# Kernel optimization log

Hardware: AMD Instinct MI355X
Metric: run time of the kernel (lower is better)

## Reference

```python
import jax, jax.numpy as jnp
import numpy as np

T = 64      # simulation_length
B = 128     # batch
D = 2048    # flattened input dim / axons per core
N = 2048    # neurons per core
L = 4       # number of cores (chain, latency = index)
OUT = 1024  # number of output_sources


def setup_inputs() -> dict:
    key = jax.random.key(0)
    k0, k1, k2, k3 = jax.random.split(key, 4)
    x = jax.random.uniform(k0, (B, D), dtype=jnp.float32)          # rate-coded input in [0,1)
    # core_params[l] = core_matrix.transpose() -> shape [N, A]; scaled for sane membrane dynamics
    W = jax.random.normal(k1, (L, N, D), dtype=jnp.float32) * 0.05
    thresholds = jnp.ones((L,), dtype=jnp.float32)
    # axon_sources: per-core irregular gather indices into previous core's neurons (input for l=0)
    axon_idx = jax.random.randint(k2, (L, D), 0, D, dtype=jnp.int32)
    out_idx = jax.random.randint(k3, (OUT,), 0, N, dtype=jnp.int32)
    return dict(x=x, W=W, thresholds=thresholds, axon_idx=axon_idx,
                out_idx=out_idx, simulation_length=T)


def _ideal_spike_scan(avg, thr, T):
    """Per-cycle: m += avg; spike = (m > thr); m[m > thr] -= thr.  avg: [B, N]."""
    def step(m, _):
        m = m + avg
        s = (m > thr).astype(m.dtype)
        return m - thr * s, s
    _, spikes = jax.lax.scan(step, jnp.zeros_like(avg), None, length=T)
    return spikes  # [T, B, N]


def reference(x, W, thresholds, axon_idx, out_idx, simulation_length):
    T = simulation_length
    L = W.shape[0]
    # generate_input_spike_train: x replicated across all cycles -> cache[-1]
    prev = jnp.broadcast_to(x, (T,) + x.shape)  # [T, B, D]
    for l in range(L):
        # get_signal_tensor: gather axon source signals for every cycle
        gathered = prev[:, :, axon_idx[l]]                    # [T, B, A]
        # per-cycle matmul: torch.matmul(core_params, sig.T).T == sig @ W[l].T
        val = jnp.einsum('tba,na->tbn', gathered, W[l])       # [T, B, N]
        avg = val.mean(axis=0)                                # avg_values [B, N]
        # ideal membrane integrate + threshold-reset recurrence -> out spike train
        prev = _ideal_spike_scan(avg, thresholds[l], T)       # [T, B, N]
    # output_signals: sum of output-source spikes over all cycles
    return prev[:, :, out_idx].sum(axis=0)                    # [B, OUT]
```

## Files before the change

### kernel.cpp

```cpp
#include <hip/hip_runtime.h>

#define BB   128
#define DD   2048
#define NN   2048
#define LL   4
#define OUTN 1024
#define JBQ  32
#define NDIG 5

typedef double double4v __attribute__((ext_vector_type(4)));
typedef int    int4v    __attribute__((ext_vector_type(4)));
typedef char   char4v   __attribute__((ext_vector_type(4)));

__global__ __launch_bounds__(256) void gather0_kernel(
    const float* __restrict__ x, const int* __restrict__ idx0,
    float* __restrict__ At)
{
    int i = blockIdx.x * 256 + threadIdx.x;
    int k = i >> 7;
    int b = i & 127;
    At[i] = x[b * DD + idx0[k]];
}

__global__ __launch_bounds__(256) void wdig5_kernel(
    const float* __restrict__ W1, signed char* __restrict__ Wd)
{
    const size_t DP = (size_t)NN * DD;
    size_t i  = (size_t)blockIdx.x * 256 + threadIdx.x;
    int    l  = (int)(i / (DP / 4));
    size_t e4 = i - (size_t)l * (DP / 4);
    int n = (int)(e4 >> 9);
    int k = (int)(e4 & 511) * 4;
    float4 w = *(const float4*)(W1 + (size_t)l * DP + (size_t)n * DD + k);
    const float wv[4] = {w.x, w.y, w.z, w.w};
    unsigned long long V[4];
    #pragma unroll
    for (int e = 0; e < 4; ++e)
        V[e] = (unsigned long long)(__double2ll_rn((double)wv[e] * 0x1p33)
                                    + (1LL << 34));
    signed char* base = Wd + (size_t)l * 5 * DP
                      + (size_t)(n >> 5) * 65536 + (size_t)(k >> 6) * 2048
                      + (n & 31) * 64 + (k & 63);
    #pragma unroll
    for (int j = 0; j < NDIG; ++j) {
        char4v p = { (char)((V[0] >> (7 * j)) & 127),
                     (char)((V[1] >> (7 * j)) & 127),
                     (char)((V[2] >> (7 * j)) & 127),
                     (char)((V[3] >> (7 * j)) & 127) };
        *(char4v*)(base + (size_t)j * DP) = p;
    }
}

__global__ __launch_bounds__(256) void gather8_kernel(
    const signed char* __restrict__ c8T, const int* __restrict__ idx,
    signed char* __restrict__ g8T)
{
    int i = blockIdx.x * 256 + threadIdx.x;
    int b = i >> 9;
    int k = (i & 511) * 4;
    int4 id = *(const int4*)(idx + k);
    const signed char* row = c8T + (size_t)b * DD;
    char4v v = { row[id.x], row[id.y], row[id.z], row[id.w] };
    *(char4v*)(g8T + (size_t)(k >> 6) * 8192 + b * 64 + (k & 63)) = v;
}

__global__ __launch_bounds__(256, 2) void layer_kernel(
    const float* __restrict__ srcT,
    const int*   __restrict__ idx,
    const float* __restrict__ Wl,
    const float* __restrict__ thresholds, int l,
    const int*   __restrict__ Tptr,
    float* __restrict__ dst, signed char* __restrict__ c8T, int isLast)
{
    __shared__ double red[4 * 64 * 8];

    const int t    = threadIdx.x;
    const int wq   = t >> 6;
    const int lane = t & 63;
    const int q    = lane >> 4;
    const int c    = lane & 15;

    const int g     = blockIdx.x;
    const int btile = (g >> 3) & 7;
    const int nsup  = (g & 7) | ((g >> 6) << 3);
    const int n0    = nsup * 32;
    const int bcol  = btile * 16 + c;

    double4v pr = {0., 0., 0., 0.}, pcv = {0., 0., 0., 0.};
    pr  = __builtin_amdgcn_mfma_f64_16x16x4f64(0.25 * (double)c, 1.0, pr, 0, 0, 0);
    pcv = __builtin_amdgcn_mfma_f64_16x16x4f64(0.25, (double)c, pcv, 0, 0, 0);
    int rowD[4], colD[4];
    #pragma unroll
    for (int r = 0; r < 4; ++r) {
        rowD[r] = (int)(pr[r] + 0.25);
        colD[r] = (int)(pcv[r] + 0.25);
    }

    double4v acc0[4] = {{0.,0.,0.,0.},{0.,0.,0.,0.},{0.,0.,0.,0.},{0.,0.,0.,0.}};
    double4v acc1[4] = {{0.,0.,0.,0.},{0.,0.,0.,0.},{0.,0.,0.,0.},{0.,0.,0.,0.}};

    const int    kbase = wq * (DD / 4);
    const float* wb0   = Wl + (size_t)(n0 + c) * DD + kbase + 4 * q;
    const float* wb1   = wb0 + (size_t)16 * DD;
    const int*   ibase = idx ? (idx + kbase + 4 * q) : nullptr;

    float4 wv0[4], wv1[4];
    float4 sv[4];
    int4   iv[4];

    #pragma unroll
    for (int p = 0; p < 4; ++p) {
        wv0[p] = *(const float4*)(wb0 + 16 * p);
        wv1[p] = *(const float4*)(wb1 + 16 * p);
    }
    #pragma unroll
    for (int p = 0; p < 4; ++p) {
        int r0, r1, r2, r3;
        if (ibase) {
            int4 iv0 = *(const int4*)(ibase + 16 * p);
            r0 = iv0.x; r1 = iv0.y; r2 = iv0.z; r3 = iv0.w;
        } else {
            int kb = kbase + 16 * p + 4 * q;
            r0 = kb; r1 = kb + 1; r2 = kb + 2; r3 = kb + 3;
        }
        sv[p].x = srcT[(size_t)r0 * BB + bcol];
        sv[p].y = srcT[(size_t)r1 * BB + bcol];
        sv[p].z = srcT[(size_t)r2 * BB + bcol];
        sv[p].w = srcT[(size_t)r3 * BB + bcol];
    }
    if (ibase) {
        #pragma unroll
        for (int p = 0; p < 4; ++p) iv[p] = *(const int4*)(ibase + 16 * (4 + p));
    }

    for (int u = 0; u < JBQ / 4; ++u) {
        #pragma unroll
        for (int gg = 0; gg < 4; ++gg) {
            float4 w0 = wv0[gg];
            float4 w1 = wv1[gg];
            float4 s  = sv[gg];

            int jn = 4 * u + 4 + gg; if (jn > JBQ - 1) jn = JBQ - 1;
            wv0[gg] = *(const float4*)(wb0 + 16 * jn);
            wv1[gg] = *(const float4*)(wb1 + 16 * jn);

            int r0, r1, r2, r3;
            if (ibase) {
                int4 ivv = iv[gg];
                r0 = ivv.x; r1 = ivv.y; r2 = ivv.z; r3 = ivv.w;
            } else {
                int kb = kbase + 16 * jn + 4 * q;
                r0 = kb; r1 = kb + 1; r2 = kb + 2; r3 = kb + 3;
            }
            sv[gg].x = srcT[(size_t)r0 * BB + bcol];
            sv[gg].y = srcT[(size_t)r1 * BB + bcol];
            sv[gg].z = srcT[(size_t)r2 * BB + bcol];
            sv[gg].w = srcT[(size_t)r3 * BB + bcol];

            if (ibase) {
                int jm = 4 * u + 8 + gg; if (jm > JBQ - 1) jm = JBQ - 1;
                iv[gg] = *(const int4*)(ibase + 16 * jm);
            }

            acc0[0] = __builtin_amdgcn_mfma_f64_16x16x4f64((double)w0.x, (double)s.x, acc0[0], 0, 0, 0);
            acc1[0] = __builtin_amdgcn_mfma_f64_16x16x4f64((double)w1.x, (double)s.x, acc1[0], 0, 0, 0);
            acc0[1] = __builtin_amdgcn_mfma_f64_16x16x4f64((double)w0.y, (double)s.y, acc0[1], 0, 0, 0);
            acc1[1] = __builtin_amdgcn_mfma_f64_16x16x4f64((double)w1.y, (double)s.y, acc1[1], 0, 0, 0);
            acc0[2] = __builtin_amdgcn_mfma_f64_16x16x4f64((double)w0.z, (double)s.z, acc0[2], 0, 0, 0);
            acc1[2] = __builtin_amdgcn_mfma_f64_16x16x4f64((double)w1.z, (double)s.z, acc1[2], 0, 0, 0);
            acc0[3] = __builtin_amdgcn_mfma_f64_16x16x4f64((double)w0.w, (double)s.w, acc0[3], 0, 0, 0);
            acc1[3] = __builtin_amdgcn_mfma_f64_16x16x4f64((double)w1.w, (double)s.w, acc1[3], 0, 0, 0);
        }
    }

    double4v a0 = (acc0[0] + acc0[1]) + (acc0[2] + acc0[3]);
    double4v a1 = (acc1[0] + acc1[1]) + (acc1[2] + acc1[3]);

    {
        double* my = red + ((size_t)wq * 64 + lane) * 8;
        #pragma unroll
        for (int r = 0; r < 4; ++r) { my[r] = a0[r]; my[4 + r] = a1[r]; }
    }
    __syncthreads();
    if (wq < 2) {
        const int off = wq * 4;
        double a[4];
        #pragma unroll
        for (int r = 0; r < 4; ++r) {
            a[r] =  red[((size_t)0 * 64 + lane) * 8 + off + r];
            a[r] += red[((size_t)1 * 64 + lane) * 8 + off + r];
            a[r] += red[((size_t)2 * 64 + lane) * 8 + off + r];
            a[r] += red[((size_t)3 * 64 + lane) * 8 + off + r];
        }

        const double th = (double)thresholds[l];
        const int T = *Tptr;
        const float sc = isLast ? 1.0f : (1.0f / (float)T);
        double m0 = 0., m1 = 0., m2 = 0., m3 = 0.;
        int c0 = 0, c1 = 0, c2 = 0, c3 = 0;
        for (int tt = 0; tt < T; ++tt) {
            m0 += a[0]; if (m0 > th) { c0++; m0 -= th; }
            m1 += a[1]; if (m1 > th) { c1++; m1 -= th; }
            m2 += a[2]; if (m2 > th) { c2++; m2 -= th; }
            m3 += a[3]; if (m3 > th) { c3++; m3 -= th; }
        }
        int cnt[4] = {c0, c1, c2, c3};
        #pragma unroll
        for (int r = 0; r < 4; ++r) {
            int n = n0 + 16 * wq + rowD[r];
            int b = btile * 16 + colD[r];
            dst[(size_t)n * BB + b] = (float)cnt[r] * sc;
            if (c8T) c8T[(size_t)b * NN + n] = (signed char)cnt[r];
        }
    }
}

__global__ __launch_bounds__(256, 2) void layer_i8_kernel(
    const signed char* __restrict__ B8,
    const signed char* __restrict__ Wd5,
    const float* __restrict__ thresholds, int l,
    const int*   __restrict__ Tptr,
    float* __restrict__ dst, signed char* __restrict__ c8T, int isLast)
{
    __shared__ double red[4 * 64 * 8];

    const int t    = threadIdx.x;
    const int wq   = t >> 6;
    const int lane = t & 63;
    const int q    = lane >> 4;
    const int c    = lane & 15;

    const int g     = blockIdx.x;
    const int btile = (g >> 3) & 7;
    const int nsup  = (g & 7) | ((g >> 6) << 3);
    const int n0    = nsup * 32;
    const int bcol  = btile * 16 + c;

    int rowD[4], colD[4];
    {
        const int cb  = c * 0x01010101;
        const int hot = (q == 0) ? 1 : 0;
        int4v aLab = {cb, cb, cb, cb};
        int4v oneh = {hot, 0, 0, 0};
        int4v dR = {0, 0, 0, 0}, dC = {0, 0, 0, 0};
        dR = __builtin_amdgcn_mfma_i32_16x16x64_i8(aLab, oneh, dR, 0, 0, 0);
        dC = __builtin_amdgcn_mfma_i32_16x16x64_i8(oneh, aLab, dC, 0, 0, 0);
        #pragma unroll
        for (int r = 0; r < 4; ++r) { rowD[r] = dR[r]; colD[r] = dC[r]; }
    }

    int4v acc0[NDIG], acc1[NDIG], accS = (int4v)0;
    #pragma unroll
    for (int j = 0; j < NDIG; ++j) { acc0[j] = (int4v)0; acc1[j] = (int4v)0; }

    const size_t DP = (size_t)NN * DD;
    const signed char* ab = Wd5 + (size_t)nsup * 65536 + c * 64 + q * 16;
    const signed char* bb = B8 + bcol * 64 + q * 16;

    const int4v ones = {0x01010101, 0x01010101, 0x01010101, 0x01010101};
    const int ck0 = wq * 8;

    int4v A0[NDIG], A1[NDIG], Bv;
    int4v N0[NDIG], N1[NDIG], Nb;

    {
        const signed char* ap = ab + (size_t)ck0 * 2048;
        #pragma unroll
        for (int j = 0; j < NDIG; ++j) {
            A0[j] = *(const int4v*)(ap + (size_t)j * DP);
            A1[j] = *(const int4v*)(ap + (size_t)j * DP + 1024);
        }
        Bv = *(const int4v*)(bb + (size_t)ck0 * 8192);
    }

    #pragma unroll 1
    for (int u = 0; u < 3; ++u) {
        {
            const signed char* ap = ab + (size_t)(ck0 + 2 * u + 1) * 2048;
            #pragma unroll
            for (int j = 0; j < NDIG; ++j) {
                N0[j] = *(const int4v*)(ap + (size_t)j * DP);
                N1[j] = *(const int4v*)(ap + (size_t)j * DP + 1024);
            }
            Nb = *(const int4v*)(bb + (size_t)(ck0 + 2 * u + 1) * 8192);
        }
        #pragma unroll
        for (int j = 0; j < NDIG; ++j) {
            acc0[j] = __builtin_amdgcn_mfma_i32_16x16x64_i8(A0[j], Bv, acc0[j], 0, 0, 0);
            acc1[j] = __builtin_amdgcn_mfma_i32_16x16x64_i8(A1[j], Bv, acc1[j], 0, 0, 0);
        }
        accS = __builtin_amdgcn_mfma_i32_16x16x64_i8(ones, Bv, accS, 0, 0, 0);
        {
            const signed char* ap = ab + (size_t)(ck0 + 2 * u + 2) * 2048;
            #pragma unroll
            for (int j = 0; j < NDIG; ++j) {
                A0[j] = *(const int4v*)(ap + (size_t)j * DP);
                A1[j] = *(const int4v*)(ap + (size_t)j * DP + 1024);
            }
            Bv = *(const int4v*)(bb + (size_t)(ck0 + 2 * u + 2) * 8192);
        }
        #pragma unroll
        for (int j = 0; j < NDIG; ++j) {
            acc0[j] = __builtin_amdgcn_mfma_i32_16x16x64_i8(N0[j], Nb, acc0[j], 0, 0, 0);
            acc1[j] = __builtin_amdgcn_mfma_i32_16x16x64_i8(N1[j], Nb, acc1[j], 0, 0, 0);
        }
        accS = __builtin_amdgcn_mfma_i32_16x16x64_i8(ones, Nb, accS, 0, 0, 0);
    }
    {
        const signed char* ap = ab + (size_t)(ck0 + 7) * 2048;
        #pragma unroll
        for (int j = 0; j < NDIG; ++j) {
            N0[j] = *(const int4v*)(ap + (size_t)j * DP);
            N1[j] = *(const int4v*)(ap + (size_t)j * DP + 1024);
        }
        Nb = *(const int4v*)(bb + (size_t)(ck0 + 7) * 8192);
    }
    #pragma unroll
    for (int j = 0; j < NDIG; ++j) {
        acc0[j] = __builtin_amdgcn_mfma_i32_16x16x64_i8(A0[j], Bv, acc0[j], 0, 0, 0);
        acc1[j] = __builtin_amdgcn_mfma_i32_16x16x64_i8(A1[j], Bv, acc1[j], 0, 0, 0);
    }
    accS = __builtin_amdgcn_mfma_i32_16x16x64_i8(ones, Bv, accS, 0, 0, 0);
    #pragma unroll
    for (int j = 0; j < NDIG; ++j) {
        acc0[j] = __builtin_amdgcn_mfma_i32_16x16x64_i8(N0[j], Nb, acc0[j], 0, 0, 0);
        acc1[j] = __builtin_amdgcn_mfma_i32_16x16x64_i8(N1[j], Nb, acc1[j], 0, 0, 0);
    }
    accS = __builtin_amdgcn_mfma_i32_16x16x64_i8(ones, Nb, accS, 0, 0, 0);

    const double S0 = 0x1p-33, S1 = 0x1p-26, S2 = 0x1p-19,
                 S3 = 0x1p-12, S4 = 0x1p-5;
    {
        double* my = red + ((size_t)wq * 64 + lane) * 8;
        #pragma unroll
        for (int r = 0; r < 4; ++r) {
            double corr = 2.0 * (double)accS[r];
            my[r]     = S0 * (double)acc0[0][r] + S1 * (double)acc0[1][r]
                      + S2 * (double)acc0[2][r] + S3 * (double)acc0[3][r]
                      + S4 * (double)acc0[4][r] - corr;
            my[4 + r] = S0 * (double)acc1[0][r] + S1 * (double)acc1[1][r]
                      + S2 * (double)acc1[2][r] + S3 * (double)acc1[3][r]
                      + S4 * (double)acc1[4][r] - corr;
        }
    }
    __syncthreads();
    if (wq < 2) {
        const int off = wq * 4;
        double a[4];
        #pragma unroll
        for (int r = 0; r < 4; ++r) {
            a[r] =  red[((size_t)0 * 64 + lane) * 8 + off + r];
            a[r] += red[((size_t)1 * 64 + lane) * 8 + off + r];
            a[r] += red[((size_t)2 * 64 + lane) * 8 + off + r];
            a[r] += red[((size_t)3 * 64 + lane) * 8 + off + r];
        }

        const double th = (double)thresholds[l];
        const int T = *Tptr;
        const double invT = 1.0 / (double)T;
        const float sc = isLast ? 1.0f : (1.0f / (float)T);
        double m0 = 0., m1 = 0., m2 = 0., m3 = 0.;
        int c0 = 0, c1 = 0, c2 = 0, c3 = 0;
        const double v0 = a[0] * invT, v1 = a[1] * invT,
                     v2 = a[2] * invT, v3 = a[3] * invT;
        for (int tt = 0; tt < T; ++tt) {
            m0 += v0; if (m0 > th) { c0++; m0 -= th; }
            m1 += v1; if (m1 > th) { c1++; m1 -= th; }
            m2 += v2; if (m2 > th) { c2++; m2 -= th; }
            m3 += v3; if (m3 > th) { c3++; m3 -= th; }
        }
        int cnt[4] = {c0, c1, c2, c3};
        #pragma unroll
        for (int r = 0; r < 4; ++r) {
            int n = n0 + 16 * wq + rowD[r];
            int b = btile * 16 + colD[r];
            dst[(size_t)n * BB + b] = (float)cnt[r] * sc;
            if (c8T) c8T[(size_t)b * NN + n] = (signed char)cnt[r];
        }
    }
}

__global__ __launch_bounds__(256) void out_kernel(
    const float* __restrict__ cntT, const int* __restrict__ out_idx,
    float* __restrict__ out)
{
    int i = blockIdx.x * 256 + threadIdx.x;
    int b = i >> 10;
    int o = i & 1023;
    out[i] = cntT[(size_t)out_idx[o] * BB + b];
}

extern "C" void kernel_launch(void* const* d_in, const int* in_sizes, int n_in,
                              void* d_out, int out_size, void* d_ws, size_t ws_size,
                              hipStream_t stream)
{
    const float* x    = (const float*)d_in[0];
    const float* W    = (const float*)d_in[1];
    const float* thr  = (const float*)d_in[2];
    const int*   axon = (const int*)d_in[3];
    const int*   oidx = (const int*)d_in[4];
    const int*   Tptr = (const int*)d_in[5];
    float* out = (float*)d_out;

    const size_t DP = (size_t)NN * DD;
    char* ws = (char*)d_ws;
    float* At   = (float*)ws;
    float* mA   = (float*)(ws + (1u << 20));
    float* mB   = (float*)(ws + (2u << 20));
    float* cntT = (float*)(ws + (3u << 20));
    signed char* c8A = (signed char*)(ws + (4u << 20));
    signed char* c8B = (signed char*)(ws + (4u << 20) + (256u << 10));
    signed char* g8T = (signed char*)(ws + (4u << 20) + (512u << 10));
    signed char* Wd  = (signed char*)(ws + (5u << 20));

    const int useI8 = (ws_size >= ((size_t)80 << 20)) ? 1 : 0;

    gather0_kernel<<<(DD * BB) / 256, 256, 0, stream>>>(x, axon, At);

    if (!useI8) {
        const float* srcs[LL] = { At, mA, mB, mA };
        float*       dsts[LL] = { mA, mB, mA, cntT };
        for (int l = 0; l < LL; ++l) {
            const int* idx = (l == 0) ? nullptr : (axon + (size_t)l * DD);
            layer_kernel<<<512, 256, 0, stream>>>(
                srcs[l], idx, W + (size_t)l * NN * DD, thr, l, Tptr,
                dsts[l], nullptr, (l == LL - 1) ? 1 : 0);
        }
    } else {
        wdig5_kernel<<<(int)(3 * (DP / 4) / 256), 256, 0, stream>>>(W + DP, Wd);

        layer_kernel<<<512, 256, 0, stream>>>(
            At, nullptr, W, thr, 0, Tptr, mA, c8A, 0);

        signed char* c8s[3] = { c8A, c8B, c8A };
        signed char* c8d[3] = { c8B, c8A, nullptr };
        float*       fds[3] = { mB, mA, cntT };
        for (int l = 1; l < LL; ++l) {
            gather8_kernel<<<(BB * DD / 4) / 256, 256, 0, stream>>>(
                c8s[l - 1], axon + (size_t)l * DD, g8T);
            layer_i8_kernel<<<512, 256, 0, stream>>>(
                g8T, Wd + (size_t)(l - 1) * 5 * DP, thr, l, Tptr,
                fds[l - 1], c8d[l - 1], (l == LL - 1) ? 1 : 0);
        }
    }

    out_kernel<<<(BB * OUTN) / 256, 256, 0, stream>>>(cntT, oidx, out);
}
```

Before: 215.4 us.

## Fuse axon gathers into layer kernels and drop standalone gather launches

The layer-0 input gather now happens inside layer_kernel: it reads x directly through the axon index with stride parameters, so the transposed staging buffer and its kernel are gone. The int8 layers now gather the previous layer's spike counts into a shared-memory B tile at block start, replacing the separate gather8 kernel and its global round trip. The goal is to cut four kernel launches and intermediate global traffic. In exchange, every block redundantly gathers its batch tile, layer-0 reads from x are strided rather than coalesced, LDS use per block grows, and the fallback path no longer launches out_kernel.

```diff
diff --git a/kernel.cpp b/kernel.cpp
--- a/kernel.cpp
+++ b/kernel.cpp
@@ -11,16 +11,6 @@
 typedef double double4v __attribute__((ext_vector_type(4)));
 typedef int    int4v    __attribute__((ext_vector_type(4)));
 typedef char   char4v   __attribute__((ext_vector_type(4)));
-
-__global__ __launch_bounds__(256) void gather0_kernel(
-    const float* __restrict__ x, const int* __restrict__ idx0,
-    float* __restrict__ At)
-{
-    int i = blockIdx.x * 256 + threadIdx.x;
-    int k = i >> 7;
-    int b = i & 127;
-    At[i] = x[b * DD + idx0[k]];
-}
 
 __global__ __launch_bounds__(256) void wdig5_kernel(
     const float* __restrict__ W1, signed char* __restrict__ Wd)
@@ -51,22 +41,10 @@
     }
 }
 
-__global__ __launch_bounds__(256) void gather8_kernel(
-    const signed char* __restrict__ c8T, const int* __restrict__ idx,
-    signed char* __restrict__ g8T)
-{
-    int i = blockIdx.x * 256 + threadIdx.x;
-    int b = i >> 9;
-    int k = (i & 511) * 4;
-    int4 id = *(const int4*)(idx + k);
-    const signed char* row = c8T + (size_t)b * DD;
-    char4v v = { row[id.x], row[id.y], row[id.z], row[id.w] };
-    *(char4v*)(g8T + (size_t)(k >> 6) * 8192 + b * 64 + (k & 63)) = v;
-}
-
 __global__ __launch_bounds__(256, 2) void layer_kernel(
-    const float* __restrict__ srcT,
+    const float* __restrict__ src,
     const int*   __restrict__ idx,
+    int sR, int sB,
     const float* __restrict__ Wl,
     const float* __restrict__ thresholds, int l,
     const int*   __restrict__ Tptr,
@@ -85,6 +63,7 @@
     const int nsup  = (g & 7) | ((g >> 6) << 3);
     const int n0    = nsup * 32;
     const int bcol  = btile * 16 + c;
+    const size_t bo = (size_t)bcol * sB;
 
     double4v pr = {0., 0., 0., 0.}, pcv = {0., 0., 0., 0.};
     pr  = __builtin_amdgcn_mfma_f64_16x16x4f64(0.25 * (double)c, 1.0, pr, 0, 0, 0);
@@ -123,10 +102,10 @@
             int kb = kbase + 16 * p + 4 * q;
             r0 = kb; r1 = kb + 1; r2 = kb + 2; r3 = kb + 3;
         }
-        sv[p].x = srcT[(size_t)r0 * BB + bcol];
-        sv[p].y = srcT[(size_t)r1 * BB + bcol];
-        sv[p].z = srcT[(size_t)r2 * BB + bcol];
-        sv[p].w = srcT[(size_t)r3 * BB + bcol];
+        sv[p].x = src[(size_t)r0 * sR + bo];
+        sv[p].y = src[(size_t)r1 * sR + bo];
+        sv[p].z = src[(size_t)r2 * sR + bo];
+        sv[p].w = src[(size_t)r3 * sR + bo];
     }
     if (ibase) {
         #pragma unroll
@@ -152,10 +131,10 @@
                 int kb = kbase + 16 * jn + 4 * q;
                 r0 = kb; r1 = kb + 1; r2 = kb + 2; r3 = kb + 3;
             }
-            sv[gg].x = srcT[(size_t)r0 * BB + bcol];
-            sv[gg].y = srcT[(size_t)r1 * BB + bcol];
-            sv[gg].z = srcT[(size_t)r2 * BB + bcol];
-            sv[gg].w = srcT[(size_t)r3 * BB + bcol];
+            sv[gg].x = src[(size_t)r0 * sR + bo];
+            sv[gg].y = src[(size_t)r1 * sR + bo];
+            sv[gg].z = src[(size_t)r2 * sR + bo];
+            sv[gg].w = src[(size_t)r3 * sR + bo];
 
             if (ibase) {
                 int jm = 4 * u + 8 + gg; if (jm > JBQ - 1) jm = JBQ - 1;
@@ -216,13 +195,16 @@
 }
 
 __global__ __launch_bounds__(256, 2) void layer_i8_kernel(
-    const signed char* __restrict__ B8,
+    const signed char* __restrict__ c8,
+    const int*   __restrict__ idx,
     const signed char* __restrict__ Wd5,
     const float* __restrict__ thresholds, int l,
     const int*   __restrict__ Tptr,
     float* __restrict__ dst, signed char* __restrict__ c8T, int isLast)
 {
     __shared__ double red[4 * 64 * 8];
+    alignas(16) __shared__ signed char btl[32 * 16 * 64];
+    alignas(16) __shared__ int kidx[DD];
 
     const int t    = threadIdx.x;
     const int wq   = t >> 6;
@@ -234,7 +216,25 @@
     const int btile = (g >> 3) & 7;
     const int nsup  = (g & 7) | ((g >> 6) << 3);
     const int n0    = nsup * 32;
-    const int bcol  = btile * 16 + c;
+
+    {
+        const int4* ip = (const int4*)idx;
+        int4* kp = (int4*)kidx;
+        kp[t]       = ip[t];
+        kp[t + 256] = ip[t + 256];
+    }
+    __syncthreads();
+    {
+        const int b = t >> 4, m = t & 15;
+        const signed char* c8row = c8 + (size_t)(btile * 16 + b) * NN;
+        #pragma unroll 4
+        for (int j = 0; j < 32; ++j) {
+            int4 id = *(const int4*)(kidx + m * 4 + j * 64);
+            char4v v = { c8row[id.x], c8row[id.y], c8row[id.z], c8row[id.w] };
+            *(char4v*)(btl + j * 1024 + b * 64 + m * 4) = v;
+        }
+    }
+    __syncthreads();
 
     int rowD[4], colD[4];
     {
@@ -255,13 +255,13 @@
 
     const size_t DP = (size_t)NN * DD;
     const signed char* ab = Wd5 + (size_t)nsup * 65536 + c * 64 + q * 16;
-    const signed char* bb = B8 + bcol * 64 + q * 16;
+    const signed char* bb = btl + c * 64 + q * 16;
 
     const int4v ones = {0x01010101, 0x01010101, 0x01010101, 0x01010101};
     const int ck0 = wq * 8;
 
-    int4v A0[NDIG], A1[NDIG], Bv;
-    int4v N0[NDIG], N1[NDIG], Nb;
+    int4v A0[NDIG], A1[NDIG];
+    int4v N0[NDIG], N1[NDIG];
 
     {
         const signed char* ap = ab + (size_t)ck0 * 2048;
@@ -270,7 +270,6 @@
             A0[j] = *(const int4v*)(ap + (size_t)j * DP);
             A1[j] = *(const int4v*)(ap + (size_t)j * DP + 1024);
         }
-        Bv = *(const int4v*)(bb + (size_t)ck0 * 8192);
     }
 
     #pragma unroll 1
@@ -282,14 +281,16 @@
                 N0[j] = *(const int4v*)(ap + (size_t)j * DP);
                 N1[j] = *(const int4v*)(ap + (size_t)j * DP + 1024);
             }
-            Nb = *(const int4v*)(bb + (size_t)(ck0 + 2 * u + 1) * 8192);
-        }
-        #pragma unroll
-        for (int j = 0; j < NDIG; ++j) {
-            acc0[j] = __builtin_amdgcn_mfma_i32_16x16x64_i8(A0[j], Bv, acc0[j], 0, 0, 0);
-            acc1[j] = __builtin_amdgcn_mfma_i32_16x16x64_i8(A1[j], Bv, acc1[j], 0, 0, 0);
-        }
-        accS = __builtin_amdgcn_mfma_i32_16x16x64_i8(ones, Bv, accS, 0, 0, 0);
+        }
+        {
+            int4v Bv = *(const int4v*)(bb + (size_t)(ck0 + 2 * u) * 1024);
+            #pragma unroll
+            for (int j = 0; j < NDIG; ++j) {
+                acc0[j] = __builtin_amdgcn_mfma_i32_16x16x64_i8(A0[j], Bv, acc0[j], 0, 0, 0);
+                acc1[j] = __builtin_amdgcn_mfma_i32_16x16x64_i8(A1[j], Bv, acc1[j], 0, 0, 0);
+            }
+            accS = __builtin_amdgcn_mfma_i32_16x16x64_i8(ones, Bv, accS, 0, 0, 0);
+        }
         {
             const signed char* ap = ab + (size_t)(ck0 + 2 * u + 2) * 2048;
             #pragma unroll
@@ -297,14 +298,16 @@
                 A0[j] = *(const int4v*)(ap + (size_t)j * DP);
                 A1[j] = *(const int4v*)(ap + (size_t)j * DP + 1024);
             }
-            Bv = *(const int4v*)(bb + (size_t)(ck0 + 2 * u + 2) * 8192);
-        }
-        #pragma unroll
-        for (int j = 0; j < NDIG; ++j) {
-            acc0[j] = __builtin_amdgcn_mfma_i32_16x16x64_i8(N0[j], Nb, acc0[j], 0, 0, 0);
-            acc1[j] = __builtin_amdgcn_mfma_i32_16x16x64_i8(N1[j], Nb, acc1[j], 0, 0, 0);
-        }
-        accS = __builtin_amdgcn_mfma_i32_16x16x64_i8(ones, Nb, accS, 0, 0, 0);
+        }
+        {
+            int4v Bv = *(const int4v*)(bb + (size_t)(ck0 + 2 * u + 1) * 1024);
+            #pragma unroll
+            for (int j = 0; j < NDIG; ++j) {
+                acc0[j] = __builtin_amdgcn_mfma_i32_16x16x64_i8(N0[j], Bv, acc0[j], 0, 0, 0);
+                acc1[j] = __builtin_amdgcn_mfma_i32_16x16x64_i8(N1[j], Bv, acc1[j], 0, 0, 0);
+            }
+            accS = __builtin_amdgcn_mfma_i32_16x16x64_i8(ones, Bv, accS, 0, 0, 0);
+        }
     }
     {
         const signed char* ap = ab + (size_t)(ck0 + 7) * 2048;
@@ -313,20 +316,25 @@
             N0[j] = *(const int4v*)(ap + (size_t)j * DP);
             N1[j] = *(const int4v*)(ap + (size_t)j * DP + 1024);
         }
-        Nb = *(const int4v*)(bb + (size_t)(ck0 + 7) * 8192);
-    }
-    #pragma unroll
-    for (int j = 0; j < NDIG; ++j) {
-        acc0[j] = __builtin_amdgcn_mfma_i32_16x16x64_i8(A0[j], Bv, acc0[j], 0, 0, 0);
-        acc1[j] = __builtin_amdgcn_mfma_i32_16x16x64_i8(A1[j], Bv, acc1[j], 0, 0, 0);
-    }
-    accS = __builtin_amdgcn_mfma_i32_16x16x64_i8(ones, Bv, accS, 0, 0, 0);
-    #pragma unroll
-    for (int j = 0; j < NDIG; ++j) {
-        acc0[j] = __builtin_amdgcn_mfma_i32_16x16x64_i8(N0[j], Nb, acc0[j], 0, 0, 0);
-        acc1[j] = __builtin_amdgcn_mfma_i32_16x16x64_i8(N1[j], Nb, acc1[j], 0, 0, 0);
-    }
-    accS = __builtin_amdgcn_mfma_i32_16x16x64_i8(ones, Nb, accS, 0, 0, 0);
+    }
+    {
+        int4v Bv = *(const int4v*)(bb + (size_t)(ck0 + 6) * 1024);
+        #pragma unroll
+        for (int j = 0; j < NDIG; ++j) {
+            acc0[j] = __builtin_amdgcn_mfma_i32_16x16x64_i8(A0[j], Bv, acc0[j], 0, 0, 0);
+            acc1[j] = __builtin_amdgcn_mfma_i32_16x16x64_i8(A1[j], Bv, acc1[j], 0, 0, 0);
+        }
+        accS = __builtin_amdgcn_mfma_i32_16x16x64_i8(ones, Bv, accS, 0, 0, 0);
+    }
+    {
+        int4v Bv = *(const int4v*)(bb + (size_t)(ck0 + 7) * 1024);
+        #pragma unroll
+        for (int j = 0; j < NDIG; ++j) {
+            acc0[j] = __builtin_amdgcn_mfma_i32_16x16x64_i8(N0[j], Bv, acc0[j], 0, 0, 0);
+            acc1[j] = __builtin_amdgcn_mfma_i32_16x16x64_i8(N1[j], Bv, acc1[j], 0, 0, 0);
+        }
+        accS = __builtin_amdgcn_mfma_i32_16x16x64_i8(ones, Bv, accS, 0, 0, 0);
+    }
 
     const double S0 = 0x1p-33, S1 = 0x1p-26, S2 = 0x1p-19,
                  S3 = 0x1p-12, S4 = 0x1p-5;
@@ -404,45 +412,38 @@
 
     const size_t DP = (size_t)NN * DD;
     char* ws = (char*)d_ws;
-    float* At   = (float*)ws;
     float* mA   = (float*)(ws + (1u << 20));
     float* mB   = (float*)(ws + (2u << 20));
     float* cntT = (float*)(ws + (3u << 20));
     signed char* c8A = (signed char*)(ws + (4u << 20));
     signed char* c8B = (signed char*)(ws + (4u << 20) + (256u << 10));
-    signed char* g8T = (signed char*)(ws + (4u << 20) + (512u << 10));
     signed char* Wd  = (signed char*)(ws + (5u << 20));
 
     const int useI8 = (ws_size >= ((size_t)80 << 20)) ? 1 : 0;
 
-    gather0_kernel<<<(DD * BB) / 256, 256, 0, stream>>>(x, axon, At);
-
     if (!useI8) {
-        const float* srcs[LL] = { At, mA, mB, mA };
+        const float* srcs[LL] = { x, mA, mB, mA };
         float*       dsts[LL] = { mA, mB, mA, cntT };
         for (int l = 0; l < LL; ++l) {
-            const int* idx = (l == 0) ? nullptr : (axon + (size_t)l * DD);
             layer_kernel<<<512, 256, 0, stream>>>(
-                srcs[l], idx, W + (size_t)l * NN * DD, thr, l, Tptr,
+                srcs[l], axon + (size_t)l * DD,
+                (l == 0) ? 1 : BB, (l == 0) ? DD : 1,
+                W + (size_t)l * NN * DD, thr, l, Tptr,
                 dsts[l], nullptr, (l == LL - 1) ? 1 : 0);
         }
     } else {
         wdig5_kernel<<<(int)(3 * (DP / 4) / 256), 256, 0, stream>>>(W + DP, Wd);
 
         layer_kernel<<<512, 256, 0, stream>>>(
-            At, nullptr, W, thr, 0, Tptr, mA, c8A, 0);
-
-        signed char* c8s[3] = { c8A, c8B, c8A };
-        signed char* c8d[3] = { c8B, c8A, nullptr };
-        float*       fds[3] = { mB, mA, cntT };
-        for (int l = 1; l < LL; ++l) {
-            gather8_kernel<<<(BB * DD / 4) / 256, 256, 0, stream>>>(
-                c8s[l - 1], axon + (size_t)l * DD, g8T);
-            layer_i8_kernel<<<512, 256, 0, stream>>>(
-                g8T, Wd + (size_t)(l - 1) * 5 * DP, thr, l, Tptr,
-                fds[l - 1], c8d[l - 1], (l == LL - 1) ? 1 : 0);
-        }
-    }
-
-    out_kernel<<<(BB * OUTN) / 256, 256, 0, stream>>>(cntT, oidx, out);
+            x, axon, 1, DD, W, thr, 0, Tptr, mA, c8A, 0);
+
+        layer_i8_kernel<<<512, 256, 0, stream>>>(
+            c8A, axon + 1 * DD, Wd + 0 * 5 * DP, thr, 1, Tptr, mB, c8B, 0);
+        layer_i8_kernel<<<512, 256, 0, stream>>>(
+            c8B, axon + 2 * DD, Wd + 1 * 5 * DP, thr, 2, Tptr, mA, c8A, 0);
+        layer_i8_kernel<<<512, 256, 0, stream>>>(
+            c8A, axon + 3 * DD, Wd + 2 * 5 * DP, thr, 3, Tptr, cntT, nullptr, 1);
+
+        out_kernel<<<(BB * OUTN) / 256, 256, 0, stream>>>(cntT, oidx, out);
+    }
 }
```

Result: slower. 265.1 us (+23.1%).
